# Performance work log

Measured on AMD Instinct MI355X. Metric: run time of the kernel, lower is better.

Reference implementation:

```python
import jax, jax.numpy as jnp
import numpy as np


def _gru_layer(x, h0, W_ih, W_hh, b_ih, b_hh):
    """PyTorch-convention GRU layer.
    x: [B, T, F], h0: [B, H], W_ih: [3H, F], W_hh: [3H, H], biases: [3H].
    Gate order (torch): r, z, n.  Returns (out [B,T,H], hT [B,H]).
    """
    # Precompute input projections for all timesteps in one big GEMM.
    gx = jnp.einsum('btf,gf->btg', x, W_ih) + b_ih  # [B, T, 3H]
    gx = jnp.swapaxes(gx, 0, 1)  # [T, B, 3H] for scan

    def step(h, gx_t):
        gh = h @ W_hh.T + b_hh                      # [B, 3H]
        xr, xz, xn = jnp.split(gx_t, 3, axis=-1)
        hr, hz, hn = jnp.split(gh, 3, axis=-1)
        r = jax.nn.sigmoid(xr + hr)
        z = jax.nn.sigmoid(xz + hz)
        n = jnp.tanh(xn + r * hn)
        h_new = (1.0 - z) * n + z * h
        return h_new, h_new

    hT, outs = jax.lax.scan(step, h0, gx)
    return jnp.swapaxes(outs, 0, 1), hT  # [B, T, H], [B, H]


def setup_inputs() -> dict:
    key = jax.random.key(0)
    ks = jax.random.split(key, 12)
    B, T, F, H, O = 256, 2000, 80, 64, 29
    s = 1.0 / np.sqrt(H)  # torch GRU/Linear init scale ~ U(-1/sqrt(H), 1/sqrt(H))
    u = lambda k, shp: jax.random.uniform(k, shp, jnp.float32, -s, s)
    return {
        'x': jax.random.normal(ks[0], (B, T, F), jnp.float32),
        'h': jnp.zeros((2, B, H), jnp.float32),
        'W_ih0': u(ks[1], (3 * H, F)),
        'W_hh0': u(ks[2], (3 * H, H)),
        'b_ih0': u(ks[3], (3 * H,)),
        'b_hh0': u(ks[4], (3 * H,)),
        'W_ih1': u(ks[5], (3 * H, H)),
        'W_hh1': u(ks[6], (3 * H, H)),
        'b_ih1': u(ks[7], (3 * H,)),
        'b_hh1': u(ks[8], (3 * H,)),
        'W_fc': u(ks[9], (O, H)),
        'b_fc': u(ks[10], (O,)),
    }


def reference(x, h, W_ih0, W_hh0, b_ih0, b_hh0, W_ih1, W_hh1, b_ih1, b_hh1, W_fc, b_fc):
    # Layer 0
    out0, h0T = _gru_layer(x, h[0], W_ih0, W_hh0, b_ih0, b_hh0)
    # Layer 1 (inter-layer dropout disabled: inference / eval mode)
    out1, h1T = _gru_layer(out0, h[1], W_ih1, W_hh1, b_ih1, b_hh1)
    hidden_state = jnp.stack([h0T, h1T], axis=0)  # [num_layers, B, H]
    # fc(relu(output[:, -1]))
    logits = jax.nn.relu(out1[:, -1]) @ W_fc.T + b_fc  # [B, O]
    return logits, hidden_state
```

## Files before the change

kernel.cpp:

```cpp
#include <hip/hip_runtime.h>

#define T_STEPS 2000
#define BATCH   256
#define F_IN    80
#define HDIM    64

template<int N> struct IC { static constexpr int v = N; };

typedef _Float16 h2 __attribute__((ext_vector_type(2)));
typedef _Float16 h4 __attribute__((ext_vector_type(4)));
typedef _Float16 h8 __attribute__((ext_vector_type(8)));

union U8 { h8 v; h2 p[4]; };
union U4 { h4 v; h2 p[2]; };

__device__ __forceinline__ float sigm_f(float v) {
    float e = __expf(-v);
    return __builtin_amdgcn_rcpf(1.f + e);
}
__device__ __forceinline__ float tanh_f(float v) {
    v = fminf(fmaxf(v, -15.f), 15.f);
    float e = __expf(-2.f * v);
    return (1.f - e) * __builtin_amdgcn_rcpf(1.f + e);
}
__device__ __forceinline__ float qred(float v) {
    v += __int_as_float(__builtin_amdgcn_mov_dpp(__float_as_int(v), 0xB1, 0xF, 0xF, true));
    v += __int_as_float(__builtin_amdgcn_mov_dpp(__float_as_int(v), 0x4E, 0xF, 0xF, true));
    return v;
}
__device__ __forceinline__ void barrier_lds() {
    __builtin_amdgcn_s_waitcnt(0xC07F);
    __builtin_amdgcn_s_barrier();
}
__device__ __forceinline__ float fdot2(h2 a, h2 b, float c) {
    return __builtin_amdgcn_fdot2(a, b, c, false);
}
__device__ __forceinline__ h2 mk2(float a, float b) {
    h2 r; r.x = (_Float16)a; r.y = (_Float16)b; return r;
}

__global__ __launch_bounds__(512, 2)
void gru_fused(const float* __restrict__ x,
               const float* __restrict__ hin,
               const float* __restrict__ Wih0,
               const float* __restrict__ Whh0,
               const float* __restrict__ bih0, const float* __restrict__ bhh0,
               const float* __restrict__ Wih1,
               const float* __restrict__ Whh1,
               const float* __restrict__ bih1, const float* __restrict__ bhh1,
               float* __restrict__ out_hidden)
{
    const int b    = blockIdx.x;
    const int tid  = threadIdx.x;
    const int lane = tid & 63;
    const int w    = tid >> 6;
    const bool isL1 = (w >= 4);
    const int ks   = lane & 3;
    const int gg   = lane >> 2;
    const int jw   = ((w & 3) << 4) + gg;

    __shared__ __align__(16) _Float16 xsh[2][96];
    __shared__ __align__(16) _Float16 h0s[2][64];
    __shared__ __align__(16) _Float16 h1s[2][64];

    h2 wxr[10], wxz[10], wxn[10];
    h2 whr[8],  whz[8],  whn[8];
    float bihr, bihz, bihn, bhhr, bhhz, bhhn;
    if (!isL1) {
        const int c = ks * 20, c2 = ks * 16;
        const float* r0 = Wih0 + jw * F_IN + c;
        const float* r1 = Wih0 + (64 + jw) * F_IN + c;
        const float* r2 = Wih0 + (128 + jw) * F_IN + c;
        #pragma unroll
        for (int k = 0; k < 10; ++k) {
            wxr[k] = mk2(r0[2*k], r0[2*k+1]);
            wxz[k] = mk2(r1[2*k], r1[2*k+1]);
            wxn[k] = mk2(r2[2*k], r2[2*k+1]);
        }
        const float* s0 = Whh0 + jw * HDIM + c2;
        const float* s1 = Whh0 + (64 + jw) * HDIM + c2;
        const float* s2 = Whh0 + (128 + jw) * HDIM + c2;
        #pragma unroll
        for (int k = 0; k < 8; ++k) {
            whr[k] = mk2(s0[2*k], s0[2*k+1]);
            whz[k] = mk2(s1[2*k], s1[2*k+1]);
            whn[k] = mk2(s2[2*k], s2[2*k+1]);
        }
        bihr = bih0[jw];       bhhr = bhh0[jw];
        bihz = bih0[64 + jw];  bhhz = bhh0[64 + jw];
        bihn = bih0[128 + jw]; bhhn = bhh0[128 + jw];
    } else {
        const int c2 = ks * 16;
        const float* r0 = Wih1 + jw * HDIM + c2;
        const float* r1 = Wih1 + (64 + jw) * HDIM + c2;
        const float* r2 = Wih1 + (128 + jw) * HDIM + c2;
        const float* s0 = Whh1 + jw * HDIM + c2;
        const float* s1 = Whh1 + (64 + jw) * HDIM + c2;
        const float* s2 = Whh1 + (128 + jw) * HDIM + c2;
        #pragma unroll
        for (int k = 0; k < 8; ++k) {
            wxr[k] = mk2(r0[2*k], r0[2*k+1]);
            wxz[k] = mk2(r1[2*k], r1[2*k+1]);
            wxn[k] = mk2(r2[2*k], r2[2*k+1]);
            whr[k] = mk2(s0[2*k], s0[2*k+1]);
            whz[k] = mk2(s1[2*k], s1[2*k+1]);
            whn[k] = mk2(s2[2*k], s2[2*k+1]);
        }
        wxr[8] = mk2(0.f, 0.f); wxr[9] = mk2(0.f, 0.f);
        wxz[8] = mk2(0.f, 0.f); wxz[9] = mk2(0.f, 0.f);
        wxn[8] = mk2(0.f, 0.f); wxn[9] = mk2(0.f, 0.f);
        bihr = bih1[jw] + bhh1[jw];
        bihz = bih1[64 + jw] + bhh1[64 + jw];
        bihn = bih1[128 + jw];
        bhhn = bhh1[128 + jw];
        bhhr = 0.f; bhhz = 0.f;
    }

    float hreg = isL1 ? hin[BATCH * HDIM + b * HDIM + jw]
                      : hin[b * HDIM + jw];
    if (w == 0) {
        h0s[1][lane] = (_Float16)hin[b * HDIM + lane];
        h1s[1][lane] = (_Float16)hin[BATCH * HDIM + b * HDIM + lane];
    }
    const float* xrow = x + (size_t)b * T_STEPS * F_IN;
    const int xe = 2 * lane;
    const int xc = xe / 20, xpp = xe % 20;
    float2 xa = make_float2(0.f, 0.f), xb = make_float2(0.f, 0.f);
    if (w == 7 && lane < 40) {
        float2 v0 = ((const float2*)(xrow + 0 * F_IN))[lane];
        float2 v1 = ((const float2*)(xrow + 1 * F_IN))[lane];
        *(h2*)(&xsh[0][xc * 24 + xpp]) = mk2(v0.x, v0.y);
        *(h2*)(&xsh[1][xc * 24 + xpp]) = mk2(v1.x, v1.y);
        xa = ((const float2*)(xrow + 2 * F_IN))[lane];
        xb = ((const float2*)(xrow + 3 * F_IN))[lane];
    }
    __syncthreads();

    float gxr = 0.f, gxz = 0.f, gxn = 0.f;
    if (!isL1) {
        U8 x0, x1; U4 x2;
        x0.v = ((const h8*)(&xsh[0][ks * 24]))[0];
        x1.v = ((const h8*)(&xsh[0][ks * 24]))[1];
        x2.v = *(const h4*)(&xsh[0][ks * 24 + 16]);
        float ar = 0.f, az = 0.f, an = 0.f;
        #pragma unroll
        for (int q = 0; q < 4; ++q) {
            ar = fdot2(wxr[q], x0.p[q], ar);
            az = fdot2(wxz[q], x0.p[q], az);
            an = fdot2(wxn[q], x0.p[q], an);
        }
        #pragma unroll
        for (int q = 0; q < 4; ++q) {
            ar = fdot2(wxr[4 + q], x1.p[q], ar);
            az = fdot2(wxz[4 + q], x1.p[q], az);
            an = fdot2(wxn[4 + q], x1.p[q], an);
        }
        #pragma unroll
        for (int q = 0; q < 2; ++q) {
            ar = fdot2(wxr[8 + q], x2.p[q], ar);
            az = fdot2(wxz[8 + q], x2.p[q], az);
            an = fdot2(wxn[8 + q], x2.p[q], an);
        }
        gxr = qred(ar) + bihr; gxz = qred(az) + bihz; gxn = qred(an) + bihn;
    }

    auto step = [&](int i, auto ipc) {
        constexpr int IP = decltype(ipc)::v;
        constexpr int IO = IP ^ 1;

        if (w == 7 && lane < 40) {
            float2 v = (IP == 0) ? xa : xb;
            *(h2*)(&xsh[IP][xc * 24 + xpp]) = mk2(v.x, v.y);
            if (i <= T_STEPS - 5) {
                float2 nv = ((const float2*)(xrow + (size_t)(i + 4) * F_IN))[lane];
                if (IP == 0) xa = nv; else xb = nv;
            }
        }

        if (!isL1) {
            U8 ha, hb;
            ha.v = ((const h8*)(&h0s[IO][ks * 16]))[0];
            hb.v = ((const h8*)(&h0s[IO][ks * 16]))[1];
            U8 x0, x1; U4 x2;
            x0.v = ((const h8*)(&xsh[IO][ks * 24]))[0];
            x1.v = ((const h8*)(&xsh[IO][ks * 24]))[1];
            x2.v = *(const h4*)(&xsh[IO][ks * 24 + 16]);

            float ahr = 0.f, ahz = 0.f, ahn = 0.f;
            #pragma unroll
            for (int q = 0; q < 4; ++q) {
                ahr = fdot2(whr[q], ha.p[q], ahr);
                ahz = fdot2(whz[q], ha.p[q], ahz);
                ahn = fdot2(whn[q], ha.p[q], ahn);
            }
            #pragma unroll
            for (int q = 0; q < 4; ++q) {
                ahr = fdot2(whr[4 + q], hb.p[q], ahr);
                ahz = fdot2(whz[4 + q], hb.p[q], ahz);
                ahn = fdot2(whn[4 + q], hb.p[q], ahn);
            }
            float r = sigm_f(gxr + qred(ahr) + bhhr);
            float z = sigm_f(gxz + qred(ahz) + bhhz);
            float n = tanh_f(gxn + r * (qred(ahn) + bhhn));
            hreg = (1.f - z) * n + z * hreg;
            if (ks == 0) h0s[IP][jw] = (_Float16)hreg;

            float axr = 0.f, axz = 0.f, axn = 0.f;
            #pragma unroll
            for (int q = 0; q < 4; ++q) {
                axr = fdot2(wxr[q], x0.p[q], axr);
                axz = fdot2(wxz[q], x0.p[q], axz);
                axn = fdot2(wxn[q], x0.p[q], axn);
            }
            #pragma unroll
            for (int q = 0; q < 4; ++q) {
                axr = fdot2(wxr[4 + q], x1.p[q], axr);
                axz = fdot2(wxz[4 + q], x1.p[q], axz);
                axn = fdot2(wxn[4 + q], x1.p[q], axn);
            }
            #pragma unroll
            for (int q = 0; q < 2; ++q) {
                axr = fdot2(wxr[8 + q], x2.p[q], axr);
                axz = fdot2(wxz[8 + q], x2.p[q], axz);
                axn = fdot2(wxn[8 + q], x2.p[q], axn);
            }
            gxr = qred(axr) + bihr;
            gxz = qred(axz) + bihz;
            gxn = qred(axn) + bihn;
        } else if (i >= 1) {
            U8 aa, ab, ba, bb;
            aa.v = ((const h8*)(&h0s[IO][ks * 16]))[0];
            ab.v = ((const h8*)(&h0s[IO][ks * 16]))[1];
            ba.v = ((const h8*)(&h1s[IP][ks * 16]))[0];
            bb.v = ((const h8*)(&h1s[IP][ks * 16]))[1];
            float ar = 0.f, az = 0.f, anx = 0.f, anh = 0.f;
            #pragma unroll
            for (int q = 0; q < 4; ++q) {
                ar  = fdot2(wxr[q], aa.p[q], ar);
                az  = fdot2(wxz[q], aa.p[q], az);
                anx = fdot2(wxn[q], aa.p[q], anx);
            }
            #pragma unroll
            for (int q = 0; q < 4; ++q) {
                ar  = fdot2(wxr[4 + q], ab.p[q], ar);
                az  = fdot2(wxz[4 + q], ab.p[q], az);
                anx = fdot2(wxn[4 + q], ab.p[q], anx);
            }
            #pragma unroll
            for (int q = 0; q < 4; ++q) {
                ar  = fdot2(whr[q], ba.p[q], ar);
                az  = fdot2(whz[q], ba.p[q], az);
                anh = fdot2(whn[q], ba.p[q], anh);
            }
            #pragma unroll
            for (int q = 0; q < 4; ++q) {
                ar  = fdot2(whr[4 + q], bb.p[q], ar);
                az  = fdot2(whz[4 + q], bb.p[q], az);
                anh = fdot2(whn[4 + q], bb.p[q], anh);
            }
            float r = sigm_f(qred(ar) + bihr);
            float z = sigm_f(qred(az) + bihz);
            float n = tanh_f(qred(anx) + bihn + r * (qred(anh) + bhhn));
            hreg = (1.f - z) * n + z * hreg;
            if (ks == 0) h1s[IO][jw] = (_Float16)hreg;
        }

        barrier_lds();
    };

    for (int ii = 0; ii < T_STEPS / 2; ++ii) {
        step(2 * ii,     IC<0>{});
        step(2 * ii + 1, IC<1>{});
    }

    if (isL1) {
        U8 aa, ab, ba, bb;
        aa.v = ((const h8*)(&h0s[1][ks * 16]))[0];
        ab.v = ((const h8*)(&h0s[1][ks * 16]))[1];
        ba.v = ((const h8*)(&h1s[0][ks * 16]))[0];
        bb.v = ((const h8*)(&h1s[0][ks * 16]))[1];
        float ar = 0.f, az = 0.f, anx = 0.f, anh = 0.f;
        #pragma unroll
        for (int q = 0; q < 4; ++q) {
            ar  = fdot2(wxr[q], aa.p[q], ar);
            az  = fdot2(wxz[q], aa.p[q], az);
            anx = fdot2(wxn[q], aa.p[q], anx);
        }
        #pragma unroll
        for (int q = 0; q < 4; ++q) {
            ar  = fdot2(wxr[4 + q], ab.p[q], ar);
            az  = fdot2(wxz[4 + q], ab.p[q], az);
            anx = fdot2(wxn[4 + q], ab.p[q], anx);
        }
        #pragma unroll
        for (int q = 0; q < 4; ++q) {
            ar  = fdot2(whr[q], ba.p[q], ar);
            az  = fdot2(whz[q], ba.p[q], az);
            anh = fdot2(whn[q], ba.p[q], anh);
        }
        #pragma unroll
        for (int q = 0; q < 4; ++q) {
            ar  = fdot2(whr[4 + q], bb.p[q], ar);
            az  = fdot2(whz[4 + q], bb.p[q], az);
            anh = fdot2(whn[4 + q], bb.p[q], anh);
        }
        float r = sigm_f(qred(ar) + bihr);
        float z = sigm_f(qred(az) + bihz);
        float n = tanh_f(qred(anx) + bihn + r * (qred(anh) + bhhn));
        hreg = (1.f - z) * n + z * hreg;
    }

    if (ks == 0) {
        if (!isL1) out_hidden[b * HDIM + jw] = hreg;
        else       out_hidden[BATCH * HDIM + b * HDIM + jw] = hreg;
    }
}

__global__ void fc_kernel(const float* __restrict__ hidden,
                          const float* __restrict__ Wfc,
                          const float* __restrict__ bfc,
                          float* __restrict__ logits)
{
    const int b = blockIdx.x;
    const int o = threadIdx.x;
    if (o < 29) {
        const float* hb = hidden + BATCH * HDIM + b * HDIM;
        float acc = bfc[o];
        #pragma unroll
        for (int j = 0; j < HDIM; ++j)
            acc += fmaxf(hb[j], 0.f) * Wfc[o * HDIM + j];
        logits[b * 29 + o] = acc;
    }
}

extern "C" void kernel_launch(void* const* d_in, const int* in_sizes, int n_in,
                              void* d_out, int out_size, void* d_ws, size_t ws_size,
                              hipStream_t stream) {
    const float* x    = (const float*)d_in[0];
    const float* h    = (const float*)d_in[1];
    const float* Wih0 = (const float*)d_in[2];
    const float* Whh0 = (const float*)d_in[3];
    const float* bih0 = (const float*)d_in[4];
    const float* bhh0 = (const float*)d_in[5];
    const float* Wih1 = (const float*)d_in[6];
    const float* Whh1 = (const float*)d_in[7];
    const float* bih1 = (const float*)d_in[8];
    const float* bhh1 = (const float*)d_in[9];
    const float* Wfc  = (const float*)d_in[10];
    const float* bfc  = (const float*)d_in[11];

    float* out    = (float*)d_out;
    float* logits = out;
    float* hidden = out + BATCH * 29;

    gru_fused<<<BATCH, 512, 0, stream>>>(
        x, h, Wih0, Whh0, bih0, bhh0, Wih1, Whh1, bih1, bhh1, hidden);

    fc_kernel<<<BATCH, 64, 0, stream>>>(hidden, Wfc, bfc, logits);
}
```

Baseline: 1.247 ms.

## Precompute layer-0 input projections in a separate GEMM kernel before recurrence

Adds a prep kernel that converts Wih0 to fp16 and folds the biases, plus a per-row gx_gemm kernel that writes fp16 input-gate projections for all timesteps into the workspace. The recurrent kernel is templated so that layer 0 reads these precomputed gates from global memory with two-step prefetch, instead of computing the x projection on its critical path each step. This removes per-step fdot2 work and the x staging through LDS. In exchange it writes and reads about 200 MB of fp16 intermediates, launches 512k small blocks, and falls back to the old path when the workspace is too small.

New measurement: 1.977 ms. 58.6% more time.

```diff
diff --git a/kernel.cpp b/kernel.cpp
--- a/kernel.cpp
+++ b/kernel.cpp
@@ -39,8 +39,50 @@
     h2 r; r.x = (_Float16)a; r.y = (_Float16)b; return r;
 }
 
+__global__ void prep_kernel(const float* __restrict__ Wih0,
+                            const float* __restrict__ bih0,
+                            const float* __restrict__ bhh0,
+                            _Float16* __restrict__ Wh2,
+                            float* __restrict__ bias_ext)
+{
+    int i = blockIdx.x * blockDim.x + threadIdx.x;
+    if (i < 192 * F_IN) Wh2[i] = (_Float16)Wih0[i];
+    if (i < 192)        bias_ext[i] = bih0[i] + (i < 128 ? bhh0[i] : 0.f);
+}
+
+__global__ __launch_bounds__(192)
+void gx_gemm(const float* __restrict__ x,
+             const _Float16* __restrict__ Wh2,
+             const float* __restrict__ bias_ext,
+             _Float16* __restrict__ gxp)
+{
+    const int r = blockIdx.x;
+    const int c = threadIdx.x;
+    __shared__ __align__(16) _Float16 xs[F_IN];
+    const float* xr = x + (size_t)r * F_IN;
+    if (c < 40) {
+        float2 v = ((const float2*)xr)[c];
+        *(h2*)(&xs[2 * c]) = mk2(v.x, v.y);
+    }
+    __syncthreads();
+    const h8* wp = (const h8*)(Wh2 + c * F_IN);
+    const h8* xp = (const h8*)xs;
+    float acc = bias_ext[c];
+    #pragma unroll
+    for (int q = 0; q < 10; ++q) {
+        U8 wq, xq;
+        wq.v = wp[q];
+        xq.v = xp[q];
+        #pragma unroll
+        for (int p = 0; p < 4; ++p) acc = fdot2(wq.p[p], xq.p[p], acc);
+    }
+    gxp[(size_t)r * 192 + c] = (_Float16)acc;
+}
+
+template<int USE_GX>
 __global__ __launch_bounds__(512, 2)
 void gru_fused(const float* __restrict__ x,
+               const _Float16* __restrict__ gx,
                const float* __restrict__ hin,
                const float* __restrict__ Wih0,
                const float* __restrict__ Whh0,
@@ -65,18 +107,9 @@
 
     h2 wxr[10], wxz[10], wxn[10];
     h2 whr[8],  whz[8],  whn[8];
-    float bihr, bihz, bihn, bhhr, bhhz, bhhn;
+    float bihr = 0.f, bihz = 0.f, bihn = 0.f, bhhr = 0.f, bhhz = 0.f, bhhn = 0.f;
     if (!isL1) {
-        const int c = ks * 20, c2 = ks * 16;
-        const float* r0 = Wih0 + jw * F_IN + c;
-        const float* r1 = Wih0 + (64 + jw) * F_IN + c;
-        const float* r2 = Wih0 + (128 + jw) * F_IN + c;
-        #pragma unroll
-        for (int k = 0; k < 10; ++k) {
-            wxr[k] = mk2(r0[2*k], r0[2*k+1]);
-            wxz[k] = mk2(r1[2*k], r1[2*k+1]);
-            wxn[k] = mk2(r2[2*k], r2[2*k+1]);
-        }
+        const int c2 = ks * 16;
         const float* s0 = Whh0 + jw * HDIM + c2;
         const float* s1 = Whh0 + (64 + jw) * HDIM + c2;
         const float* s2 = Whh0 + (128 + jw) * HDIM + c2;
@@ -86,9 +119,22 @@
             whz[k] = mk2(s1[2*k], s1[2*k+1]);
             whn[k] = mk2(s2[2*k], s2[2*k+1]);
         }
-        bihr = bih0[jw];       bhhr = bhh0[jw];
-        bihz = bih0[64 + jw];  bhhz = bhh0[64 + jw];
-        bihn = bih0[128 + jw]; bhhn = bhh0[128 + jw];
+        bhhn = bhh0[128 + jw];
+        if constexpr (USE_GX == 0) {
+            const int c = ks * 20;
+            const float* r0 = Wih0 + jw * F_IN + c;
+            const float* r1 = Wih0 + (64 + jw) * F_IN + c;
+            const float* r2 = Wih0 + (128 + jw) * F_IN + c;
+            #pragma unroll
+            for (int k = 0; k < 10; ++k) {
+                wxr[k] = mk2(r0[2*k], r0[2*k+1]);
+                wxz[k] = mk2(r1[2*k], r1[2*k+1]);
+                wxn[k] = mk2(r2[2*k], r2[2*k+1]);
+            }
+            bihr = bih0[jw];       bhhr = bhh0[jw];
+            bihz = bih0[64 + jw];  bhhz = bhh0[64 + jw];
+            bihn = bih0[128 + jw];
+        }
     } else {
         const int c2 = ks * 16;
         const float* r0 = Wih1 + jw * HDIM + c2;
@@ -113,7 +159,6 @@
         bihz = bih1[64 + jw] + bhh1[64 + jw];
         bihn = bih1[128 + jw];
         bhhn = bhh1[128 + jw];
-        bhhr = 0.f; bhhz = 0.f;
     }
 
     float hreg = isL1 ? hin[BATCH * HDIM + b * HDIM + jw]
@@ -126,54 +171,75 @@
     const int xe = 2 * lane;
     const int xc = xe / 20, xpp = xe % 20;
     float2 xa = make_float2(0.f, 0.f), xb = make_float2(0.f, 0.f);
-    if (w == 7 && lane < 40) {
-        float2 v0 = ((const float2*)(xrow + 0 * F_IN))[lane];
-        float2 v1 = ((const float2*)(xrow + 1 * F_IN))[lane];
-        *(h2*)(&xsh[0][xc * 24 + xpp]) = mk2(v0.x, v0.y);
-        *(h2*)(&xsh[1][xc * 24 + xpp]) = mk2(v1.x, v1.y);
-        xa = ((const float2*)(xrow + 2 * F_IN))[lane];
-        xb = ((const float2*)(xrow + 3 * F_IN))[lane];
-    }
+    if constexpr (USE_GX == 0) {
+        if (w == 7 && lane < 40) {
+            float2 v0 = ((const float2*)(xrow + 0 * F_IN))[lane];
+            float2 v1 = ((const float2*)(xrow + 1 * F_IN))[lane];
+            *(h2*)(&xsh[0][xc * 24 + xpp]) = mk2(v0.x, v0.y);
+            *(h2*)(&xsh[1][xc * 24 + xpp]) = mk2(v1.x, v1.y);
+            xa = ((const float2*)(xrow + 2 * F_IN))[lane];
+            xb = ((const float2*)(xrow + 3 * F_IN))[lane];
+        }
+    }
+
+    _Float16 pr0 = (_Float16)0.f, pz0 = (_Float16)0.f, pn0 = (_Float16)0.f;
+    _Float16 pr1 = (_Float16)0.f, pz1 = (_Float16)0.f, pn1 = (_Float16)0.f;
+    const _Float16* gp0 = nullptr;
+    const _Float16* gp1 = nullptr;
+    if constexpr (USE_GX) {
+        if (!isL1) {
+            const _Float16* gb = gx + (size_t)b * T_STEPS * 192 + jw;
+            pr0 = gb[0];       pz0 = gb[64];        pn0 = gb[128];
+            pr1 = gb[192];     pz1 = gb[256];       pn1 = gb[320];
+            gp0 = gb + 2 * 192;
+            gp1 = gb + 3 * 192;
+        }
+    }
+
     __syncthreads();
 
     float gxr = 0.f, gxz = 0.f, gxn = 0.f;
-    if (!isL1) {
-        U8 x0, x1; U4 x2;
-        x0.v = ((const h8*)(&xsh[0][ks * 24]))[0];
-        x1.v = ((const h8*)(&xsh[0][ks * 24]))[1];
-        x2.v = *(const h4*)(&xsh[0][ks * 24 + 16]);
-        float ar = 0.f, az = 0.f, an = 0.f;
-        #pragma unroll
-        for (int q = 0; q < 4; ++q) {
-            ar = fdot2(wxr[q], x0.p[q], ar);
-            az = fdot2(wxz[q], x0.p[q], az);
-            an = fdot2(wxn[q], x0.p[q], an);
-        }
-        #pragma unroll
-        for (int q = 0; q < 4; ++q) {
-            ar = fdot2(wxr[4 + q], x1.p[q], ar);
-            az = fdot2(wxz[4 + q], x1.p[q], az);
-            an = fdot2(wxn[4 + q], x1.p[q], an);
-        }
-        #pragma unroll
-        for (int q = 0; q < 2; ++q) {
-            ar = fdot2(wxr[8 + q], x2.p[q], ar);
-            az = fdot2(wxz[8 + q], x2.p[q], az);
-            an = fdot2(wxn[8 + q], x2.p[q], an);
-        }
-        gxr = qred(ar) + bihr; gxz = qred(az) + bihz; gxn = qred(an) + bihn;
+    if constexpr (USE_GX == 0) {
+        if (!isL1) {
+            U8 x0, x1; U4 x2;
+            x0.v = ((const h8*)(&xsh[0][ks * 24]))[0];
+            x1.v = ((const h8*)(&xsh[0][ks * 24]))[1];
+            x2.v = *(const h4*)(&xsh[0][ks * 24 + 16]);
+            float ar = 0.f, az = 0.f, an = 0.f;
+            #pragma unroll
+            for (int q = 0; q < 4; ++q) {
+                ar = fdot2(wxr[q], x0.p[q], ar);
+                az = fdot2(wxz[q], x0.p[q], az);
+                an = fdot2(wxn[q], x0.p[q], an);
+            }
+            #pragma unroll
+            for (int q = 0; q < 4; ++q) {
+                ar = fdot2(wxr[4 + q], x1.p[q], ar);
+                az = fdot2(wxz[4 + q], x1.p[q], az);
+                an = fdot2(wxn[4 + q], x1.p[q], an);
+            }
+            #pragma unroll
+            for (int q = 0; q < 2; ++q) {
+                ar = fdot2(wxr[8 + q], x2.p[q], ar);
+                az = fdot2(wxz[8 + q], x2.p[q], az);
+                an = fdot2(wxn[8 + q], x2.p[q], an);
+            }
+            gxr = qred(ar) + bihr; gxz = qred(az) + bihz; gxn = qred(an) + bihn;
+        }
     }
 
     auto step = [&](int i, auto ipc) {
         constexpr int IP = decltype(ipc)::v;
         constexpr int IO = IP ^ 1;
 
-        if (w == 7 && lane < 40) {
-            float2 v = (IP == 0) ? xa : xb;
-            *(h2*)(&xsh[IP][xc * 24 + xpp]) = mk2(v.x, v.y);
-            if (i <= T_STEPS - 5) {
-                float2 nv = ((const float2*)(xrow + (size_t)(i + 4) * F_IN))[lane];
-                if (IP == 0) xa = nv; else xb = nv;
+        if constexpr (USE_GX == 0) {
+            if (w == 7 && lane < 40) {
+                float2 v = (IP == 0) ? xa : xb;
+                *(h2*)(&xsh[IP][xc * 24 + xpp]) = mk2(v.x, v.y);
+                if (i <= T_STEPS - 5) {
+                    float2 nv = ((const float2*)(xrow + (size_t)(i + 4) * F_IN))[lane];
+                    if (IP == 0) xa = nv; else xb = nv;
+                }
             }
         }
 
@@ -182,9 +248,19 @@
             ha.v = ((const h8*)(&h0s[IO][ks * 16]))[0];
             hb.v = ((const h8*)(&h0s[IO][ks * 16]))[1];
             U8 x0, x1; U4 x2;
-            x0.v = ((const h8*)(&xsh[IO][ks * 24]))[0];
-            x1.v = ((const h8*)(&xsh[IO][ks * 24]))[1];
-            x2.v = *(const h4*)(&xsh[IO][ks * 24 + 16]);
+            if constexpr (USE_GX == 0) {
+                x0.v = ((const h8*)(&xsh[IO][ks * 24]))[0];
+                x1.v = ((const h8*)(&xsh[IO][ks * 24]))[1];
+                x2.v = *(const h4*)(&xsh[IO][ks * 24 + 16]);
+            }
+
+            float gr_f = 0.f, gz_f = 0.f, gn_f = 0.f;
+            if constexpr (USE_GX) {
+                if (IP == 0) { gr_f = (float)pr0; gz_f = (float)pz0; gn_f = (float)pn0; }
+                else         { gr_f = (float)pr1; gz_f = (float)pz1; gn_f = (float)pn1; }
+                if (IP == 0) { pr0 = gp0[0]; pz0 = gp0[64]; pn0 = gp0[128]; gp0 += 2 * 192; }
+                else         { pr1 = gp1[0]; pz1 = gp1[64]; pn1 = gp1[128]; gp1 += 2 * 192; }
+            }
 
             float ahr = 0.f, ahz = 0.f, ahn = 0.f;
             #pragma unroll
@@ -199,34 +275,43 @@
                 ahz = fdot2(whz[4 + q], hb.p[q], ahz);
                 ahn = fdot2(whn[4 + q], hb.p[q], ahn);
             }
-            float r = sigm_f(gxr + qred(ahr) + bhhr);
-            float z = sigm_f(gxz + qred(ahz) + bhhz);
-            float n = tanh_f(gxn + r * (qred(ahn) + bhhn));
+            float r, z, n;
+            if constexpr (USE_GX) {
+                r = sigm_f(gr_f + qred(ahr));
+                z = sigm_f(gz_f + qred(ahz));
+                n = tanh_f(gn_f + r * (qred(ahn) + bhhn));
+            } else {
+                r = sigm_f(gxr + qred(ahr) + bhhr);
+                z = sigm_f(gxz + qred(ahz) + bhhz);
+                n = tanh_f(gxn + r * (qred(ahn) + bhhn));
+            }
             hreg = (1.f - z) * n + z * hreg;
             if (ks == 0) h0s[IP][jw] = (_Float16)hreg;
 
-            float axr = 0.f, axz = 0.f, axn = 0.f;
-            #pragma unroll
-            for (int q = 0; q < 4; ++q) {
-                axr = fdot2(wxr[q], x0.p[q], axr);
-                axz = fdot2(wxz[q], x0.p[q], axz);
-                axn = fdot2(wxn[q], x0.p[q], axn);
-            }
-            #pragma unroll
-            for (int q = 0; q < 4; ++q) {
-                axr = fdot2(wxr[4 + q], x1.p[q], axr);
-                axz = fdot2(wxz[4 + q], x1.p[q], axz);
-                axn = fdot2(wxn[4 + q], x1.p[q], axn);
-            }
-            #pragma unroll
-            for (int q = 0; q < 2; ++q) {
-                axr = fdot2(wxr[8 + q], x2.p[q], axr);
-                axz = fdot2(wxz[8 + q], x2.p[q], axz);
-                axn = fdot2(wxn[8 + q], x2.p[q], axn);
-            }
-            gxr = qred(axr) + bihr;
-            gxz = qred(axz) + bihz;
-            gxn = qred(axn) + bihn;
+            if constexpr (USE_GX == 0) {
+                float axr = 0.f, axz = 0.f, axn = 0.f;
+                #pragma unroll
+                for (int q = 0; q < 4; ++q) {
+                    axr = fdot2(wxr[q], x0.p[q], axr);
+                    axz = fdot2(wxz[q], x0.p[q], axz);
+                    axn = fdot2(wxn[q], x0.p[q], axn);
+                }
+                #pragma unroll
+                for (int q = 0; q < 4; ++q) {
+                    axr = fdot2(wxr[4 + q], x1.p[q], axr);
+                    axz = fdot2(wxz[4 + q], x1.p[q], axz);
+                    axn = fdot2(wxn[4 + q], x1.p[q], axn);
+                }
+                #pragma unroll
+                for (int q = 0; q < 2; ++q) {
+                    axr = fdot2(wxr[8 + q], x2.p[q], axr);
+                    axz = fdot2(wxz[8 + q], x2.p[q], axz);
+                    axn = fdot2(wxn[8 + q], x2.p[q], axn);
+                }
+                gxr = qred(axr) + bihr;
+                gxz = qred(axz) + bihz;
+                gxn = qred(axn) + bihn;
+            }
         } else if (i >= 1) {
             U8 aa, ab, ba, bb;
             aa.v = ((const h8*)(&h0s[IO][ks * 16]))[0];
@@ -353,8 +438,24 @@
     float* logits = out;
     float* hidden = out + BATCH * 29;
 
-    gru_fused<<<BATCH, 512, 0, stream>>>(
-        x, h, Wih0, Whh0, bih0, bhh0, Wih1, Whh1, bih1, bhh1, hidden);
+    const size_t gx_elems = (size_t)BATCH * T_STEPS * 192 + 1024;
+    const size_t gx_bytes = gx_elems * sizeof(_Float16);
+    const size_t w_bytes  = (size_t)192 * F_IN * sizeof(_Float16);
+    const size_t need     = gx_bytes + w_bytes + 192 * sizeof(float);
+
+    if (d_ws != nullptr && ws_size >= need) {
+        _Float16* gxp      = (_Float16*)d_ws;
+        _Float16* Wh2      = (_Float16*)((char*)d_ws + gx_bytes);
+        float*    bias_ext = (float*)((char*)d_ws + gx_bytes + w_bytes);
+
+        prep_kernel<<<60, 256, 0, stream>>>(Wih0, bih0, bhh0, Wh2, bias_ext);
+        gx_gemm<<<BATCH * T_STEPS, 192, 0, stream>>>(x, Wh2, bias_ext, gxp);
+        gru_fused<1><<<BATCH, 512, 0, stream>>>(
+            x, gxp, h, Wih0, Whh0, bih0, bhh0, Wih1, Whh1, bih1, bhh1, hidden);
+    } else {
+        gru_fused<0><<<BATCH, 512, 0, stream>>>(
+            x, nullptr, h, Wih0, Whh0, bih0, bhh0, Wih1, Whh1, bih1, bhh1, hidden);
+    }
 
     fc_kernel<<<BATCH, 64, 0, stream>>>(hidden, Wfc, bfc, logits);
 }
```
